# Kernel tuning notes

Hardware: AMD Instinct MI355X
Metric: run time of the kernel (lower is better)

## Reference

```python
import jax, jax.numpy as jnp
import numpy as np

BN_EPS = 1e-5


def conv1x1(x, w, b=None):
    # x: (B,Cin,F,T), w: (Cout,Cin)
    y = jnp.einsum('oc,bcft->boft', w, x)
    if b is not None:
        y = y + b[None, :, None, None]
    return y


def maxpool2(x):
    B, C, F, T = x.shape
    return x.reshape(B, C, F // 2, 2, T // 2, 2).max(axis=(3, 5))


def pos_grid(F, T, dtype):
    # flattened (F*T,) f-position and t-position in [0,1]
    fpos = jnp.linspace(0.0, 1.0, F, dtype=dtype)
    tpos = jnp.linspace(0.0, 1.0, T, dtype=dtype)
    fg = jnp.broadcast_to(fpos[:, None], (F, T)).reshape(-1)
    tg = jnp.broadcast_to(tpos[None, :], (F, T)).reshape(-1)
    return fg, tg


def setup_inputs() -> dict:
    key = jax.random.key(0)
    ks = jax.random.split(key, 12)
    B, C, F, T = 16, 64, 64, 64
    IC = 32  # inter_channels
    s = 0.05
    inp = {
        'x': jax.random.normal(ks[0], (B, C, F, T), jnp.float32),
        'psi_w': jax.random.normal(ks[1], (IC, C), jnp.float32) * s,
        'psi_b': jax.random.normal(ks[2], (IC,), jnp.float32) * s,
        'theta_w': jax.random.normal(ks[3], (IC, C), jnp.float32) * s,
        'theta_b': jax.random.normal(ks[4], (IC,), jnp.float32) * s,
        'phi_w': jax.random.normal(ks[5], (IC, C), jnp.float32) * s,
        'phi_b': jax.random.normal(ks[6], (IC,), jnp.float32) * s,
        'concat_w': jax.random.normal(ks[7], (2 * IC + 2,), jnp.float32) * s,  # 1x1 conv, no bias
        'W_w': jax.random.normal(ks[8], (C, IC + 1), jnp.float32) * s,
        'W_b': jax.random.normal(ks[9], (C,), jnp.float32) * s,
        'bn_gamma': jax.random.normal(ks[10], (C,), jnp.float32) * s + 1.0,
        'bn_beta': jax.random.normal(ks[11], (C,), jnp.float32) * s,
    }
    return inp


def reference(x, psi_w, psi_b, theta_w, theta_b, phi_w, phi_b, concat_w, W_w, W_b, bn_gamma, bn_beta):
    B, C, F, T = x.shape
    IC = psi_w.shape[0]
    # psi / phi are sub-sampled (maxpool 2x2) per sub_sample=True
    psi = maxpool2(conv1x1(x, psi_w, psi_b))            # (B,IC,F/2,T/2)
    theta = conv1x1(x, theta_w, theta_b)                # (B,IC,F,T)
    phi = maxpool2(conv1x1(x, phi_w, phi_b))            # (B,IC,F/2,T/2)

    h = F * T
    Fp, Tp = phi.shape[2], phi.shape[3]
    w = Fp * Tp

    psi_x = psi.reshape(B, IC, w).transpose(0, 2, 1)    # (B,w,IC)
    th_flat = theta.reshape(B, IC, h)                   # (B,IC,h)
    ph_flat = phi.reshape(B, IC, w)                     # (B,IC,w)

    # concat_project is a 1x1 conv over cat([theta, phi, pos_delta]) -> score separates:
    # f[b,i,j] = relu(w_th.theta_i + w_d.pos_i + w_ph.phi_j - w_d.pos_j)
    w_th = concat_w[:IC]
    w_ph = concat_w[IC:2 * IC]
    w_d = concat_w[2 * IC:]

    fg_q, tg_q = pos_grid(F, T, x.dtype)                # (h,)
    fg_k, tg_k = pos_grid(Fp, Tp, x.dtype)              # (w,)

    a = jnp.einsum('c,bcn->bn', w_th, th_flat) + (w_d[0] * fg_q + w_d[1] * tg_q)[None, :]  # (B,h)
    c = jnp.einsum('c,bcn->bn', w_ph, ph_flat) - (w_d[0] * fg_k + w_d[1] * tg_k)[None, :]  # (B,w)

    f = jax.nn.relu(a[:, :, None] + c[:, None, :])      # (B,h,w)
    f_div_C = f / jnp.asarray(w, x.dtype)
    # note: scaled_softmax(f) feeds only calc_relation_structure; with 'zero' the
    # structure feature is zeros, so the softmax does not affect the output.

    y = jnp.matmul(f_div_C, psi_x)                      # (B,h,IC)
    y = y.transpose(0, 2, 1).reshape(B, IC, F, T)
    structure_feat = jnp.zeros((B, 1, F, T), x.dtype)   # r_structure_type='zero'
    y = jnp.concatenate([y, structure_feat], axis=1)    # (B,IC+1,F,T)

    wy = conv1x1(y, W_w, W_b)                           # (B,C,F,T)
    # BatchNorm2d, training-mode batch statistics (torch default forward)
    mean = wy.mean(axis=(0, 2, 3), keepdims=True)
    var = wy.var(axis=(0, 2, 3), keepdims=True)
    wy = (wy - mean) / jnp.sqrt(var + BN_EPS)
    wy = wy * bn_gamma[None, :, None, None] + bn_beta[None, :, None, None]

    return wy + x
```

## Files before the change

kernel.cpp:

```cpp
#include <hip/hip_runtime.h>

#define BB 16
#define CC 64
#define ICC 32
#define NN 4096
#define MM 1024

typedef __attribute__((ext_vector_type(8))) short short8;
typedef __attribute__((ext_vector_type(4))) float f32x4;

static __device__ __forceinline__ unsigned cvt_pk_bf16(float lo, float hi) {
    unsigned d;
    asm("v_cvt_pk_bf16_f32 %0, %1, %2" : "=v"(d) : "v"(lo), "v"(hi));
    return d;
}
static __device__ __forceinline__ short8 as_s8(uint4 u) {
    union { uint4 a; short8 b; } t; t.a = u; return t.b;
}
static __device__ __forceinline__ float bf16_to_f32(unsigned u) {
    return __uint_as_float(u << 16);
}

__global__ void __launch_bounds__(256) k_pool(
        const float* __restrict__ x,
        const float* __restrict__ psi_w, const float* __restrict__ psi_b,
        const float* __restrict__ phi_w, const float* __restrict__ phi_b,
        const float* __restrict__ theta_w, const float* __restrict__ theta_b,
        const float* __restrict__ concat_w,
        unsigned* __restrict__ psi_pk, float* __restrict__ c_buf,
        float* __restrict__ a_buf, float* __restrict__ sumbuf) {
    __shared__ float pw[CC * ICC];
    __shared__ float fw[CC * ICC];
    __shared__ float vth[CC];
    __shared__ float xt[CC * 64];
    __shared__ float sconst;
    int tid = threadIdx.x;
    int b = blockIdx.x >> 6;
    int mtile = blockIdx.x & 63;
    int fp = mtile >> 1;
    int tpb = (mtile & 1) * 16;

    if (blockIdx.x == 0 && tid < 2 * CC) sumbuf[tid] = 0.f;
    for (int i = tid; i < CC * ICC; i += 256) {
        int ic = i >> 6, c = i & 63;
        pw[c * ICC + ic] = psi_w[i];
        fw[c * ICC + ic] = phi_w[i];
    }
    if (tid < CC) {
        float s = 0.f;
        for (int ic = 0; ic < ICC; ++ic) s += concat_w[ic] * theta_w[ic * CC + tid];
        vth[tid] = s;
    }
    if (tid == 255) {
        float s = 0.f;
        for (int ic = 0; ic < ICC; ++ic) s += concat_w[ic] * theta_b[ic];
        sconst = s;
    }
    const float* xb = x + (size_t)b * CC * NN;
    for (int i = tid; i < 1024; i += 256) {
        int c = i >> 4, row = (i >> 3) & 1, jj = i & 7;
        float4 v = *(const float4*)(xb + c * NN + (2 * fp + row) * 64 + 2 * tpb + jj * 4);
        *(float4*)&xt[c * 64 + row * 32 + jj * 4] = v;
    }
    __syncthreads();

    int ic = tid & 31;
    int mp = tid >> 5;
    float p00=0,p01=0,p02=0,p03=0, p10=0,p11=0,p12=0,p13=0;
    float q00=0,q01=0,q02=0,q03=0, q10=0,q11=0,q12=0,q13=0;
    for (int c = 0; c < CC; ++c) {
        float4 r0 = *(const float4*)&xt[c * 64 + mp * 4];
        float4 r1 = *(const float4*)&xt[c * 64 + 32 + mp * 4];
        float wp = pw[c * ICC + ic], wf = fw[c * ICC + ic];
        p00 += wp*r0.x; p01 += wp*r0.y; p02 += wp*r1.x; p03 += wp*r1.y;
        p10 += wp*r0.z; p11 += wp*r0.w; p12 += wp*r1.z; p13 += wp*r1.w;
        q00 += wf*r0.x; q01 += wf*r0.y; q02 += wf*r1.x; q03 += wf*r1.y;
        q10 += wf*r0.z; q11 += wf*r0.w; q12 += wf*r1.z; q13 += wf*r1.w;
    }
    float pb = psi_b[ic], fb = phi_b[ic];
    float psi0 = fmaxf(fmaxf(p00,p01),fmaxf(p02,p03)) + pb;
    float psi1 = fmaxf(fmaxf(p10,p11),fmaxf(p12,p13)) + pb;
    float phi0 = fmaxf(fmaxf(q00,q01),fmaxf(q02,q03)) + fb;
    float phi1 = fmaxf(fmaxf(q10,q11),fmaxf(q12,q13)) + fb;

    int m0 = mtile * 16 + 2 * mp;
    float wd0 = concat_w[2 * ICC], wd1 = concat_w[2 * ICC + 1];
    float wph = concat_w[ICC + ic];
    float v0 = wph * phi0, v1 = wph * phi1;
    for (int off = 16; off >= 1; off >>= 1) {
        v0 += __shfl_xor(v0, off, 32);
        v1 += __shfl_xor(v1, off, 32);
    }
    if (ic == 0) {
        int tp = tpb + 2 * mp;
        c_buf[b * MM + m0]     = v0 - (wd0 * (fp * (1.f/31.f)) + wd1 * (tp * (1.f/31.f)));
        c_buf[b * MM + m0 + 1] = v1 - (wd0 * (fp * (1.f/31.f)) + wd1 * ((tp + 1) * (1.f/31.f)));
    }
    int mpg = mtile * 8 + mp;
    int ks = mpg >> 4, kg = (mpg >> 2) & 3, cidx = mpg & 3;
    psi_pk[b * 16384 + ks * 512 + (ic >> 4) * 256 + kg * 64 + (ic & 15) * 4 + cidx]
        = cvt_pk_bf16(psi0, psi1);

    if (ic < 8) {
        int pix = mp * 8 + ic;
        int row = pix >> 5, colo = pix & 31;
        float sa = 0.f;
        #pragma unroll 8
        for (int c = 0; c < CC; ++c) sa += vth[c] * xt[c * 64 + row * 32 + colo];
        int f = 2 * fp + row, t = 2 * tpb + colo;
        a_buf[b * NN + f * 64 + t] = sa + sconst + wd0 * (f * (1.f/63.f)) + wd1 * (t * (1.f/63.f));
    }
}

static __device__ __forceinline__ void mfma_step(
        int ks, const float* c_lds, int hi4, float a0, float a1,
        uint4 bu0, uint4 bu1,
        f32x4& acc00, f32x4& acc01, f32x4& acc10, f32x4& acc11) {
    float4 c0 = *(const float4*)&c_lds[ks * 32 + hi4 * 8];
    float4 c1 = *(const float4*)&c_lds[ks * 32 + hi4 * 8 + 4];
    uint4 up;
    up.x = cvt_pk_bf16(fmaxf(a0 + c0.x, 0.f), fmaxf(a0 + c0.y, 0.f));
    up.y = cvt_pk_bf16(fmaxf(a0 + c0.z, 0.f), fmaxf(a0 + c0.w, 0.f));
    up.z = cvt_pk_bf16(fmaxf(a0 + c1.x, 0.f), fmaxf(a0 + c1.y, 0.f));
    up.w = cvt_pk_bf16(fmaxf(a0 + c1.z, 0.f), fmaxf(a0 + c1.w, 0.f));
    short8 ua0 = as_s8(up);
    up.x = cvt_pk_bf16(fmaxf(a1 + c0.x, 0.f), fmaxf(a1 + c0.y, 0.f));
    up.y = cvt_pk_bf16(fmaxf(a1 + c0.z, 0.f), fmaxf(a1 + c0.w, 0.f));
    up.z = cvt_pk_bf16(fmaxf(a1 + c1.x, 0.f), fmaxf(a1 + c1.y, 0.f));
    up.w = cvt_pk_bf16(fmaxf(a1 + c1.z, 0.f), fmaxf(a1 + c1.w, 0.f));
    short8 ua1 = as_s8(up);
    short8 vb0 = as_s8(bu0), vb1 = as_s8(bu1);
    acc00 = __builtin_amdgcn_mfma_f32_16x16x32_bf16(ua0, vb0, acc00, 0, 0, 0);
    acc01 = __builtin_amdgcn_mfma_f32_16x16x32_bf16(ua0, vb1, acc01, 0, 0, 0);
    acc10 = __builtin_amdgcn_mfma_f32_16x16x32_bf16(ua1, vb0, acc10, 0, 0, 0);
    acc11 = __builtin_amdgcn_mfma_f32_16x16x32_bf16(ua1, vb1, acc11, 0, 0, 0);
}

__global__ void __launch_bounds__(256) k_attn(
        const float* __restrict__ a_buf, const float* __restrict__ c_buf,
        const unsigned* __restrict__ psi_pk,
        const float* __restrict__ W_w, const float* __restrict__ W_b,
        unsigned short* __restrict__ wy16) {
    __shared__ float c_lds[MM];
    __shared__ float W_lds[CC * ICC];
    __shared__ float Wb_lds[CC];
    __shared__ float yT[ICC * 130];
    int tid = threadIdx.x;
    int b = blockIdx.x >> 5;
    int ntile = blockIdx.x & 31;
    for (int i = tid; i < MM; i += 256) c_lds[i] = c_buf[b * MM + i];
    for (int i = tid; i < CC * ICC; i += 256) W_lds[i] = W_w[(i >> 5) * (ICC + 1) + (i & 31)];
    if (tid < CC) Wb_lds[tid] = W_b[tid];

    int w = tid >> 6, lane = tid & 63;
    int lo4 = lane & 15, hi4 = lane >> 4;
    const float* ab = a_buf + b * NN + ntile * 128 + w * 32;
    float a0 = ab[lo4], a1 = ab[16 + lo4];

    f32x4 acc00 = {0.f,0.f,0.f,0.f}, acc01 = {0.f,0.f,0.f,0.f};
    f32x4 acc10 = {0.f,0.f,0.f,0.f}, acc11 = {0.f,0.f,0.f,0.f};

    const uint4* pf4 = (const uint4*)psi_pk + (size_t)b * 4096;
    __syncthreads();

    uint4 p0a = pf4[lane],       p0b = pf4[64 + lane];
    uint4 p1a = pf4[128 + lane], p1b = pf4[192 + lane];
    for (int ks = 0; ks < 32; ks += 2) {
        uint4 n0a, n0b, n1a, n1b;
        bool more = (ks + 2 < 32);
        if (more) {
            n0a = pf4[(ks + 2) * 128 + lane]; n0b = pf4[(ks + 2) * 128 + 64 + lane];
            n1a = pf4[(ks + 3) * 128 + lane]; n1b = pf4[(ks + 3) * 128 + 64 + lane];
        }
        mfma_step(ks,     c_lds, hi4, a0, a1, p0a, p0b, acc00, acc01, acc10, acc11);
        mfma_step(ks + 1, c_lds, hi4, a0, a1, p1a, p1b, acc00, acc01, acc10, acc11);
        if (more) { p0a = n0a; p0b = n0b; p1a = n1a; p1b = n1b; }
    }

    const float inv = 1.0f / (float)MM;
    #pragma unroll
    for (int r = 0; r < 4; ++r) {
        yT[lo4 * 130 + w * 32 + hi4 * 4 + r]             = acc00[r] * inv;
        yT[(16 + lo4) * 130 + w * 32 + hi4 * 4 + r]      = acc01[r] * inv;
        yT[lo4 * 130 + w * 32 + 16 + hi4 * 4 + r]        = acc10[r] * inv;
        yT[(16 + lo4) * 130 + w * 32 + 16 + hi4 * 4 + r] = acc11[r] * inv;
    }
    __syncthreads();

    int p = tid & 127, oh = tid >> 7;
    float yv[ICC];
    #pragma unroll
    for (int icx = 0; icx < ICC; ++icx) yv[icx] = yT[icx * 130 + p];
    unsigned short* wyp = wy16 + (size_t)b * CC * NN + ntile * 128 + p;
    #pragma unroll 4
    for (int od = 0; od < 32; ++od) {
        int o = oh * 32 + od;
        float s = Wb_lds[o];
        const float* wrow = &W_lds[o * ICC];
        #pragma unroll
        for (int icx = 0; icx < ICC; ++icx) s += wrow[icx] * yv[icx];
        wyp[(size_t)o * NN] = (unsigned short)(cvt_pk_bf16(s, 0.f) & 0xffffu);
    }
}

__global__ void k_stats2(const unsigned short* __restrict__ wy16, float* __restrict__ sumbuf) {
    int o = blockIdx.x & 63, b = blockIdx.x >> 6;
    int tid = threadIdx.x;
    const uint2* p = (const uint2*)(wy16 + ((size_t)(b * CC + o)) * NN);
    float s = 0.f, s2 = 0.f;
    #pragma unroll
    for (int i = 0; i < 4; ++i) {
        uint2 v = p[tid + i * 256];
        float f0 = bf16_to_f32(v.x & 0xffffu), f1 = bf16_to_f32(v.x >> 16);
        float f2 = bf16_to_f32(v.y & 0xffffu), f3 = bf16_to_f32(v.y >> 16);
        s  += f0 + f1 + f2 + f3;
        s2 += f0*f0 + f1*f1 + f2*f2 + f3*f3;
    }
    for (int off = 32; off >= 1; off >>= 1) {
        s += __shfl_xor(s, off, 64);
        s2 += __shfl_xor(s2, off, 64);
    }
    __shared__ float ws1[4], ws2[4];
    int wv = tid >> 6;
    if ((tid & 63) == 0) { ws1[wv] = s; ws2[wv] = s2; }
    __syncthreads();
    if (tid == 0) {
        atomicAdd(&sumbuf[o], ws1[0] + ws1[1] + ws1[2] + ws1[3]);
        atomicAdd(&sumbuf[CC + o], ws2[0] + ws2[1] + ws2[2] + ws2[3]);
    }
}

__global__ void __launch_bounds__(256) k_final(
        float* __restrict__ out, const float* __restrict__ x,
        const unsigned short* __restrict__ wy16,
        const float* __restrict__ sumbuf,
        const float* __restrict__ bn_gamma, const float* __restrict__ bn_beta) {
    __shared__ float s_sc, s_sh;
    size_t i = (size_t)blockIdx.x * 256 + threadIdx.x;
    int o = (int)((i >> 10) & 63);
    if (threadIdx.x == 0) {
        float nN = (float)(BB * NN);
        float mean = sumbuf[o] / nN;
        float var = sumbuf[CC + o] / nN - mean * mean;
        float sc = bn_gamma[o] * rsqrtf(var + 1e-5f);
        s_sc = sc;
        s_sh = bn_beta[o] - mean * sc;
    }
    __syncthreads();
    float sc = s_sc, sh = s_sh;
    uint2 wv = ((const uint2*)wy16)[i];
    float4 x4 = ((const float4*)x)[i];
    float4 r;
    r.x = bf16_to_f32(wv.x & 0xffffu) * sc + sh + x4.x;
    r.y = bf16_to_f32(wv.x >> 16)     * sc + sh + x4.y;
    r.z = bf16_to_f32(wv.y & 0xffffu) * sc + sh + x4.z;
    r.w = bf16_to_f32(wv.y >> 16)     * sc + sh + x4.w;
    ((float4*)out)[i] = r;
}

extern "C" void kernel_launch(void* const* d_in, const int* in_sizes, int n_in,
                              void* d_out, int out_size, void* d_ws, size_t ws_size,
                              hipStream_t stream) {
    const float* x        = (const float*)d_in[0];
    const float* psi_w    = (const float*)d_in[1];
    const float* psi_b    = (const float*)d_in[2];
    const float* theta_w  = (const float*)d_in[3];
    const float* theta_b  = (const float*)d_in[4];
    const float* phi_w    = (const float*)d_in[5];
    const float* phi_b    = (const float*)d_in[6];
    const float* concat_w = (const float*)d_in[7];
    const float* W_w      = (const float*)d_in[8];
    const float* W_b      = (const float*)d_in[9];
    const float* bn_gamma = (const float*)d_in[10];
    const float* bn_beta  = (const float*)d_in[11];

    float* ws = (float*)d_ws;
    float*          a_buf  = ws;
    float*          c_buf  = a_buf + BB * NN;
    unsigned*       psi_pk = (unsigned*)(c_buf + BB * MM);
    float*          sumbuf = (float*)(psi_pk + BB * 16384);
    unsigned short* wy16   = (unsigned short*)(ws + 344320);
    float*          out    = (float*)d_out;

    k_pool<<<BB * 64, 256, 0, stream>>>(x, psi_w, psi_b, phi_w, phi_b,
                                        theta_w, theta_b, concat_w,
                                        psi_pk, c_buf, a_buf, sumbuf);
    k_attn<<<BB * 32, 256, 0, stream>>>(a_buf, c_buf, psi_pk, W_w, W_b, wy16);
    k_stats2<<<BB * CC, 256, 0, stream>>>(wy16, sumbuf);
    k_final<<<BB * CC * NN / 1024, 256, 0, stream>>>(out, x, wy16, sumbuf, bn_gamma, bn_beta);
}
```

Measured before the change: 136.0 us.

## Fuse BatchNorm statistics into attention kernel epilogue with per-batch partial sums

Removes the separate stats kernel, which re-read the whole bf16 wy buffer. The attention epilogue now reduces sum and sum of squares across each wavefront per output channel and atomically adds them into per-batch slots. The final kernel sums the 16 per-batch partials. This saves a launch and a full read pass, but adds 32 wave-wide shuffle reductions plus atomics per thread inside k_attn, and more atomic traffic.

```diff
diff --git a/kernel.cpp b/kernel.cpp
--- a/kernel.cpp
+++ b/kernel.cpp
@@ -40,7 +40,8 @@
     int fp = mtile >> 1;
     int tpb = (mtile & 1) * 16;
 
-    if (blockIdx.x == 0 && tid < 2 * CC) sumbuf[tid] = 0.f;
+    if (mtile == 0 && tid < 128) sumbuf[b * 128 + tid] = 0.f;
+
     for (int i = tid; i < CC * ICC; i += 256) {
         int ic = i >> 6, c = i & 63;
         pw[c * ICC + ic] = psi_w[i];
@@ -140,7 +141,7 @@
         const float* __restrict__ a_buf, const float* __restrict__ c_buf,
         const unsigned* __restrict__ psi_pk,
         const float* __restrict__ W_w, const float* __restrict__ W_b,
-        unsigned short* __restrict__ wy16) {
+        unsigned short* __restrict__ wy16, float* __restrict__ sumbuf) {
     __shared__ float c_lds[MM];
     __shared__ float W_lds[CC * ICC];
     __shared__ float Wb_lds[CC];
@@ -192,6 +193,7 @@
     #pragma unroll
     for (int icx = 0; icx < ICC; ++icx) yv[icx] = yT[icx * 130 + p];
     unsigned short* wyp = wy16 + (size_t)b * CC * NN + ntile * 128 + p;
+    float* sb = sumbuf + b * 128;
     #pragma unroll 4
     for (int od = 0; od < 32; ++od) {
         int o = oh * 32 + od;
@@ -199,34 +201,19 @@
         const float* wrow = &W_lds[o * ICC];
         #pragma unroll
         for (int icx = 0; icx < ICC; ++icx) s += wrow[icx] * yv[icx];
-        wyp[(size_t)o * NN] = (unsigned short)(cvt_pk_bf16(s, 0.f) & 0xffffu);
-    }
-}
-
-__global__ void k_stats2(const unsigned short* __restrict__ wy16, float* __restrict__ sumbuf) {
-    int o = blockIdx.x & 63, b = blockIdx.x >> 6;
-    int tid = threadIdx.x;
-    const uint2* p = (const uint2*)(wy16 + ((size_t)(b * CC + o)) * NN);
-    float s = 0.f, s2 = 0.f;
-    #pragma unroll
-    for (int i = 0; i < 4; ++i) {
-        uint2 v = p[tid + i * 256];
-        float f0 = bf16_to_f32(v.x & 0xffffu), f1 = bf16_to_f32(v.x >> 16);
-        float f2 = bf16_to_f32(v.y & 0xffffu), f3 = bf16_to_f32(v.y >> 16);
-        s  += f0 + f1 + f2 + f3;
-        s2 += f0*f0 + f1*f1 + f2*f2 + f3*f3;
-    }
-    for (int off = 32; off >= 1; off >>= 1) {
-        s += __shfl_xor(s, off, 64);
-        s2 += __shfl_xor(s2, off, 64);
-    }
-    __shared__ float ws1[4], ws2[4];
-    int wv = tid >> 6;
-    if ((tid & 63) == 0) { ws1[wv] = s; ws2[wv] = s2; }
-    __syncthreads();
-    if (tid == 0) {
-        atomicAdd(&sumbuf[o], ws1[0] + ws1[1] + ws1[2] + ws1[3]);
-        atomicAdd(&sumbuf[CC + o], ws2[0] + ws2[1] + ws2[2] + ws2[3]);
+        unsigned u = cvt_pk_bf16(s, 0.f) & 0xffffu;
+        wyp[(size_t)o * NN] = (unsigned short)u;
+        float sf = bf16_to_f32(u);
+        float s1 = sf, s2 = sf * sf;
+        #pragma unroll
+        for (int off = 32; off >= 1; off >>= 1) {
+            s1 += __shfl_xor(s1, off, 64);
+            s2 += __shfl_xor(s2, off, 64);
+        }
+        if (lane == 0) {
+            atomicAdd(&sb[o], s1);
+            atomicAdd(&sb[64 + o], s2);
+        }
     }
 }
 
@@ -239,9 +226,14 @@
     size_t i = (size_t)blockIdx.x * 256 + threadIdx.x;
     int o = (int)((i >> 10) & 63);
     if (threadIdx.x == 0) {
+        float S = 0.f, S2 = 0.f;
+        for (int bb = 0; bb < BB; ++bb) {
+            S  += sumbuf[bb * 128 + o];
+            S2 += sumbuf[bb * 128 + 64 + o];
+        }
         float nN = (float)(BB * NN);
-        float mean = sumbuf[o] / nN;
-        float var = sumbuf[CC + o] / nN - mean * mean;
+        float mean = S / nN;
+        float var = S2 / nN - mean * mean;
         float sc = bn_gamma[o] * rsqrtf(var + 1e-5f);
         s_sc = sc;
         s_sh = bn_beta[o] - mean * sc;
@@ -279,13 +271,12 @@
     float*          c_buf  = a_buf + BB * NN;
     unsigned*       psi_pk = (unsigned*)(c_buf + BB * MM);
     float*          sumbuf = (float*)(psi_pk + BB * 16384);
-    unsigned short* wy16   = (unsigned short*)(ws + 344320);
+    unsigned short* wy16   = (unsigned short*)(ws + 346112);
     float*          out    = (float*)d_out;
 
     k_pool<<<BB * 64, 256, 0, stream>>>(x, psi_w, psi_b, phi_w, phi_b,
                                         theta_w, theta_b, concat_w,
                                         psi_pk, c_buf, a_buf, sumbuf);
-    k_attn<<<BB * 32, 256, 0, stream>>>(a_buf, c_buf, psi_pk, W_w, W_b, wy16);
-    k_stats2<<<BB * CC, 256, 0, stream>>>(wy16, sumbuf);
+    k_attn<<<BB * 32, 256, 0, stream>>>(a_buf, c_buf, psi_pk, W_w, W_b, wy16, sumbuf);
     k_final<<<BB * CC * NN / 1024, 256, 0, stream>>>(out, x, wy16, sumbuf, bn_gamma, bn_beta);
 }
```

New measurement: 149.8 us. 1.1x slower.
